# Optimization experiments

Measured on AMD Instinct MI355X. Metric: run time of the kernel, lower is better.

## Reference

```python
import jax, jax.numpy as jnp
import numpy as np
import math

EMBED_DIM = 768
NUM_HEADS = 12
MLP_HIDDEN = int(EMBED_DIM * 2.0)
LN_EPS = 1e-6


def _complex_linear(r, i, wr, wi, br, bi):
    # (r + i*j) @ (wr + wi*j)^T + (br + bi*j)
    out_r = r @ wr.T - i @ wi.T + br
    out_i = r @ wi.T + i @ wr.T + bi
    return out_r, out_i


def _complex_layernorm(r, i, gamma, beta):
    # magnitude-based LN over feature dim; gamma/beta: [F, 2]
    mag = jnp.sqrt(r * r + i * i + LN_EPS)           # [..., F]
    mean = mag.mean(axis=-1, keepdims=True)
    var = ((mag - mean) ** 2).mean(axis=-1, keepdims=True)  # unbiased=False
    norm_mag = (mag - mean) / jnp.sqrt(var + LN_EPS)
    scale = norm_mag / (mag + LN_EPS)
    r_n = r * scale
    i_n = i * scale
    return gamma[..., 0] * r_n + beta[..., 0], gamma[..., 1] * i_n + beta[..., 1]


def setup_inputs() -> dict:
    key = jax.random.key(0)
    ks = jax.random.split(key, 12)
    B, N, E, H = 2, 2048, EMBED_DIM, MLP_HIDDEN
    std_qkv = math.sqrt(2.0 / (E + 3 * E))
    std_proj = math.sqrt(2.0 / (E + E))
    std_fc1 = math.sqrt(2.0 / (E + H))
    std_fc2 = math.sqrt(2.0 / (H + E))
    inp = {
        "x": jax.random.normal(ks[0], (B, N, 2 * E), dtype=jnp.float32),
        "norm1_gamma": 1.0 + 0.1 * jax.random.normal(ks[1], (E, 2), dtype=jnp.float32),
        "norm1_beta": 0.1 * jax.random.normal(ks[2], (E, 2), dtype=jnp.float32),
        "qkv_wr": std_qkv * jax.random.normal(ks[3], (3 * E, E), dtype=jnp.float32),
        "qkv_wi": std_qkv * jax.random.normal(ks[4], (3 * E, E), dtype=jnp.float32),
        "qkv_br": jnp.zeros((3 * E,), dtype=jnp.float32),
        "qkv_bi": jnp.zeros((3 * E,), dtype=jnp.float32),
        "proj_wr": std_proj * jax.random.normal(ks[5], (E, E), dtype=jnp.float32),
        "proj_wi": std_proj * jax.random.normal(ks[6], (E, E), dtype=jnp.float32),
        "proj_br": jnp.zeros((E,), dtype=jnp.float32),
        "proj_bi": jnp.zeros((E,), dtype=jnp.float32),
        "norm2_gamma": 1.0 + 0.1 * jax.random.normal(ks[7], (E, 2), dtype=jnp.float32),
        "norm2_beta": 0.1 * jax.random.normal(ks[8], (E, 2), dtype=jnp.float32),
        "fc1_wr": std_fc1 * jax.random.normal(ks[9], (H, E), dtype=jnp.float32),
        "fc1_wi": std_fc1 * jax.random.normal(ks[10], (H, E), dtype=jnp.float32),
        "fc1_br": jnp.zeros((H,), dtype=jnp.float32),
        "fc1_bi": jnp.zeros((H,), dtype=jnp.float32),
        "fc2_wr": std_fc2 * jax.random.normal(ks[11], (E, H), dtype=jnp.float32),
        "fc2_wi": std_fc2 * jax.random.normal(jax.random.fold_in(key, 99), (E, H), dtype=jnp.float32),
        "fc2_br": jnp.zeros((E,), dtype=jnp.float32),
        "fc2_bi": jnp.zeros((E,), dtype=jnp.float32),
    }
    return inp


def reference(x, norm1_gamma, norm1_beta, qkv_wr, qkv_wi, qkv_br, qkv_bi,
              proj_wr, proj_wi, proj_br, proj_bi, norm2_gamma, norm2_beta,
              fc1_wr, fc1_wi, fc1_br, fc1_bi, fc2_wr, fc2_wi, fc2_br, fc2_bi):
    B, N, _ = x.shape
    E, nH = EMBED_DIM, NUM_HEADS
    hd = E // nH
    xc = x.reshape(B, N, E, 2)
    xr, xi = xc[..., 0], xc[..., 1]

    # --- attention branch ---
    nr, ni = _complex_layernorm(xr, xi, norm1_gamma, norm1_beta)
    qkv_r, qkv_i = _complex_linear(nr, ni, qkv_wr, qkv_wi, qkv_br, qkv_bi)  # [B,N,3E]
    # split to [3, B, nH, N, hd]
    def split_heads(t):
        return t.reshape(B, N, 3, nH, hd).transpose(2, 0, 3, 1, 4)
    qkv_r = split_heads(qkv_r)
    qkv_i = split_heads(qkv_i)
    qr, kr, vr = qkv_r[0], qkv_r[1], qkv_r[2]
    qi, ki, vi = qkv_i[0], qkv_i[1], qkv_i[2]

    # complex attention scores: q * conj-free formulation per source
    attn_real = jnp.einsum('bhqd,bhkd->bhqk', qr, kr) + jnp.einsum('bhqd,bhkd->bhqk', qi, ki)
    attn_imag = jnp.einsum('bhqd,bhkd->bhqk', qr, ki) - jnp.einsum('bhqd,bhkd->bhqk', qi, kr)
    attn_mag = jnp.sqrt(attn_real ** 2 + attn_imag ** 2 + 1e-8) / math.sqrt(hd)
    attn_w = jax.nn.softmax(attn_mag, axis=-1)
    out_r = jnp.einsum('bhqk,bhkd->bhqd', attn_w, vr)
    out_i = jnp.einsum('bhqk,bhkd->bhqd', attn_w, vi)
    # [B,nH,N,hd] -> [B,N,E]
    out_r = out_r.transpose(0, 2, 1, 3).reshape(B, N, E)
    out_i = out_i.transpose(0, 2, 1, 3).reshape(B, N, E)
    pr, pi = _complex_linear(out_r, out_i, proj_wr, proj_wi, proj_br, proj_bi)
    xr = xr + pr
    xi = xi + pi

    # --- MLP branch ---
    nr2, ni2 = _complex_layernorm(xr, xi, norm2_gamma, norm2_beta)
    h_r, h_i = _complex_linear(nr2, ni2, fc1_wr, fc1_wi, fc1_br, fc1_bi)
    h_r = jax.nn.gelu(h_r, approximate=False)
    h_i = jax.nn.gelu(h_i, approximate=False)
    m_r, m_i = _complex_linear(h_r, h_i, fc2_wr, fc2_wi, fc2_br, fc2_bi)
    xr = xr + m_r
    xi = xi + m_i

    return jnp.stack([xr, xi], axis=-1).reshape(B, N, 2 * E)
```

## Files before the change

### kernel.cpp

```cpp
#include <hip/hip_runtime.h>
#include <cmath>

typedef __bf16 bf16;
typedef __bf16 bf16x8 __attribute__((ext_vector_type(8)));
typedef __bf16 bf16x4 __attribute__((ext_vector_type(4)));
typedef float  f32x4  __attribute__((ext_vector_type(4)));
typedef unsigned int u32x4 __attribute__((ext_vector_type(4)));

#define MFMA16(a, b, c) __builtin_amdgcn_mfma_f32_16x16x32_bf16((a), (b), (c), 0, 0, 0)
#define LOG2E 1.44269504088896f

static __device__ __forceinline__ void gl_lds16(const void* g, void* l) {
    __builtin_amdgcn_global_load_lds((const __attribute__((address_space(1))) void*)g,
                                     (__attribute__((address_space(3))) void*)l, 16, 0, 0);
}

static __device__ __forceinline__ bf16x8 bneg8(bf16x8 x) {
    u32x4 u = __builtin_bit_cast(u32x4, x);
    u = u ^ 0x80008000u;
    return __builtin_bit_cast(bf16x8, u);
}

static __device__ __forceinline__ f32x4 zero4() {
    return f32x4{0.0f, 0.0f, 0.0f, 0.0f};
}

__global__ void fill_kernel(float* p, float v, int n) {
    for (int i = blockIdx.x * blockDim.x + threadIdx.x; i < n; i += gridDim.x * blockDim.x)
        p[i] = v;
}

struct Cvt8 {
    const float* s[8];
    bf16* d[8];
    int boff[9];
};
__global__ __launch_bounds__(256) void cvt8_kernel(Cvt8 c) {
    int blk = blockIdx.x;
    int seg = 0;
#pragma unroll
    for (int k = 0; k < 7; ++k)
        if (blk >= c.boff[k + 1]) seg = k + 1;
    const int local = blk - c.boff[seg];
    const int i = local * 1024 + threadIdx.x * 4;
    const float4 v = *(const float4*)(c.s[seg] + i);
    bf16x4 o;
    o[0] = (bf16)v.x; o[1] = (bf16)v.y; o[2] = (bf16)v.z; o[3] = (bf16)v.w;
    *(bf16x4*)(c.d[seg] + i) = o;
}

template <bool ILV>
__global__ __launch_bounds__(256) void cln_kernel(
    const float* __restrict__ xa, const float* __restrict__ xb,
    const float* __restrict__ gamma, const float* __restrict__ beta,
    bf16* __restrict__ nr, bf16* __restrict__ ni) {
    __shared__ float red[4];
    const int t = threadIdx.x;
    const size_t base = (size_t)blockIdx.x * 768;

    float r[3], im[3], mg[3];
#pragma unroll
    for (int j = 0; j < 3; ++j) {
        const int f = t + j * 256;
        if (ILV) {
            const float2 v = ((const float2*)xa)[base + f];
            r[j] = v.x;
            im[j] = v.y;
        } else {
            r[j] = xa[base + f];
            im[j] = xb[base + f];
        }
        mg[j] = __builtin_amdgcn_sqrtf(r[j] * r[j] + im[j] * im[j] + 1e-6f);
    }
    float s = mg[0] + mg[1] + mg[2];
#pragma unroll
    for (int m = 32; m >= 1; m >>= 1) s += __shfl_xor(s, m);
    if ((t & 63) == 0) red[t >> 6] = s;
    __syncthreads();
    const float mean = (red[0] + red[1] + red[2] + red[3]) * (1.0f / 768.0f);
    __syncthreads();

    float v2 = 0.0f;
#pragma unroll
    for (int j = 0; j < 3; ++j) {
        const float d = mg[j] - mean;
        v2 += d * d;
    }
#pragma unroll
    for (int m = 32; m >= 1; m >>= 1) v2 += __shfl_xor(v2, m);
    if ((t & 63) == 0) red[t >> 6] = v2;
    __syncthreads();
    const float var = (red[0] + red[1] + red[2] + red[3]) * (1.0f / 768.0f);
    const float rstd = rsqrtf(var + 1e-6f);

#pragma unroll
    for (int j = 0; j < 3; ++j) {
        const int f = t + j * 256;
        const float sc = (mg[j] - mean) * rstd / (mg[j] + 1e-6f);
        nr[base + f] = (bf16)(gamma[2 * f] * (r[j] * sc) + beta[2 * f]);
        ni[base + f] = (bf16)(gamma[2 * f + 1] * (im[j] * sc) + beta[2 * f + 1]);
    }
}

template <int BM, int BN, int MODE, int OCC>
__global__ __launch_bounds__(256, OCC) void cgemm_kernel(
    const bf16* __restrict__ Ar, const bf16* __restrict__ Ai,
    const bf16* __restrict__ Wr, const bf16* __restrict__ Wi,
    const float* __restrict__ br, const float* __restrict__ bi,
    const float* __restrict__ resr, const float* __restrict__ resi,
    float* __restrict__ outFr, float* __restrict__ outFi,
    bf16* __restrict__ outBr, bf16* __restrict__ outBi,
    int N, int K) {
    constexpr int MR = BM / 32;
    constexpr int NR = BN / 32;
    constexpr int ASEG = BM / 8;
    constexpr int NSEG = (BM + BN) / 8;
    constexpr int SPW = NSEG / 4;

    __shared__ __align__(16) bf16 sA[2][BM][64];
    __shared__ __align__(16) bf16 sB[2][BN][64];

    const int tid = threadIdx.x;
    const int wave = tid >> 6, lane = tid & 63;
    const int lg = lane >> 4, lr = lane & 15;

    const int nwgx = gridDim.x;
    int wg = blockIdx.y * nwgx + blockIdx.x;
    const int cpx = (nwgx * gridDim.y) >> 3;
    wg = (wg & 7) * cpx + (wg >> 3);
    const int row0 = (wg % nwgx) * BM, col0 = (wg / nwgx) * BN;

    const int wm = (wave >> 1) * (BM / 2), wn = (wave & 1) * (BN / 2);

    const int srow = lane >> 3;
    const int schunk = (lane & 7) ^ srow;
    const int spl = schunk >> 2;
    const int sc8 = (schunk & 3) * 8;

    auto issue = [&](int buf, int kt) {
#pragma unroll
        for (int s = 0; s < SPW; ++s) {
            const int id = wave * SPW + s;
            if (id < ASEG) {
                const int row = id * 8 + srow;
                gl_lds16((spl ? Ai : Ar) + (size_t)(row0 + row) * K + kt + sc8,
                         &sA[buf][id * 8][0]);
            } else {
                const int row = (id - ASEG) * 8 + srow;
                gl_lds16((spl ? Wi : Wr) + (size_t)(col0 + row) * K + kt + sc8,
                         &sB[buf][(id - ASEG) * 8][0]);
            }
        }
    };

    f32x4 accr[MR][NR], acci[MR][NR];
#pragma unroll
    for (int a = 0; a < MR; ++a)
#pragma unroll
        for (int b2 = 0; b2 < NR; ++b2) {
            accr[a][b2] = zero4();
            acci[a][b2] = zero4();
        }

    issue(0, 0);

    const int KT = K / 32;
    for (int kt = 0; kt < KT; ++kt) {
        const int buf = kt & 1;
        if (kt + 1 < KT) {
            issue(buf ^ 1, (kt + 1) * 32);
            __builtin_amdgcn_sched_barrier(0);
            if constexpr (SPW == 8)
                asm volatile("s_waitcnt vmcnt(8)" ::: "memory");
            else if constexpr (SPW == 6)
                asm volatile("s_waitcnt vmcnt(6)" ::: "memory");
            else
                asm volatile("s_waitcnt vmcnt(0)" ::: "memory");
        } else {
            asm volatile("s_waitcnt vmcnt(0)" ::: "memory");
        }
        __builtin_amdgcn_sched_barrier(0);
        __builtin_amdgcn_s_barrier();
        __builtin_amdgcn_sched_barrier(0);

        __builtin_amdgcn_s_setprio(1);
        bf16x8 ar[MR], ai[MR], an[MR];
#pragma unroll
        for (int mt = 0; mt < MR; ++mt) {
            const int rr = wm + mt * 16 + lr;
            const int slr = lg ^ (rr & 7);
            const int sli = (4 + lg) ^ (rr & 7);
            ar[mt] = *(const bf16x8*)(&sA[buf][rr][slr * 8]);
            ai[mt] = *(const bf16x8*)(&sA[buf][rr][sli * 8]);
            an[mt] = bneg8(ai[mt]);
        }
#pragma unroll
        for (int nt = 0; nt < NR; ++nt) {
            const int rr = wn + nt * 16 + lr;
            const int slr = lg ^ (rr & 7);
            const int sli = (4 + lg) ^ (rr & 7);
            const bf16x8 br8 = *(const bf16x8*)(&sB[buf][rr][slr * 8]);
            const bf16x8 bi8 = *(const bf16x8*)(&sB[buf][rr][sli * 8]);
#pragma unroll
            for (int mt = 0; mt < MR; ++mt) {
                accr[mt][nt] = MFMA16(ar[mt], br8, accr[mt][nt]);
                accr[mt][nt] = MFMA16(an[mt], bi8, accr[mt][nt]);
                acci[mt][nt] = MFMA16(ar[mt], bi8, acci[mt][nt]);
                acci[mt][nt] = MFMA16(ai[mt], br8, acci[mt][nt]);
            }
        }
        __builtin_amdgcn_s_setprio(0);

        if (kt + 1 < KT) {
            __builtin_amdgcn_sched_barrier(0);
            __builtin_amdgcn_s_barrier();
            __builtin_amdgcn_sched_barrier(0);
        }
    }

#pragma unroll
    for (int nt = 0; nt < NR; ++nt) {
        const int col = col0 + wn + nt * 16 + lr;
        const float bre = br[col], bie = bi[col];
#pragma unroll
        for (int mt = 0; mt < MR; ++mt) {
#pragma unroll
            for (int j = 0; j < 4; ++j) {
                const int row = row0 + wm + mt * 16 + lg * 4 + j;
                float vr = accr[mt][nt][j] + bre;
                float vi = acci[mt][nt][j] + bie;
                const size_t o = (size_t)row * N + col;
                if (MODE == 0) {
                    outBr[o] = (bf16)vr;
                    outBi[o] = (bf16)vi;
                } else if (MODE == 1) {
                    const float2 rv = ((const float2*)resr)[(size_t)row * 768 + col];
                    outFr[o] = rv.x + vr;
                    outFi[o] = rv.y + vi;
                } else if (MODE == 2) {
                    vr = 0.5f * vr * (1.0f + erff(vr * 0.70710678118654752f));
                    vi = 0.5f * vi * (1.0f + erff(vi * 0.70710678118654752f));
                    outBr[o] = (bf16)vr;
                    outBi[o] = (bf16)vi;
                } else {
                    const size_t ro = (size_t)row * 768 + col;
                    outFr[(size_t)row * 1536 + 2 * col]     = resr[ro] + vr;
                    outFr[(size_t)row * 1536 + 2 * col + 1] = resi[ro] + vi;
                }
            }
        }
    }
}

__global__ __launch_bounds__(256) void vtrans_kernel(
    const bf16* __restrict__ qkvr, const bf16* __restrict__ qkvi,
    bf16* __restrict__ vtr, bf16* __restrict__ vti) {
    __shared__ bf16 sr[64][65];
    __shared__ bf16 si[64][65];
    const int t = threadIdx.x;
    const int nb = blockIdx.x, h = blockIdx.y, b = blockIdx.z;
    const size_t ld = 2304;
    const bf16* srcr = qkvr + (size_t)(b * 2048 + nb * 64) * ld + 1536 + h * 64;
    const bf16* srci = qkvi + (size_t)(b * 2048 + nb * 64) * ld + 1536 + h * 64;
#pragma unroll
    for (int j = 0; j < 16; ++j) {
        const int idx = t + 256 * j;
        const int n = idx >> 6, d = idx & 63;
        sr[n][d] = srcr[(size_t)n * ld + d];
        si[n][d] = srci[(size_t)n * ld + d];
    }
    __syncthreads();
    bf16* dstr = vtr + (size_t)(b * 12 + h) * 64 * 2048 + nb * 64;
    bf16* dsti = vti + (size_t)(b * 12 + h) * 64 * 2048 + nb * 64;
#pragma unroll
    for (int j = 0; j < 16; ++j) {
        const int idx = t + 256 * j;
        const int d = idx >> 6, n = idx & 63;
        dstr[(size_t)d * 2048 + n] = sr[n][d];
        dsti[(size_t)d * 2048 + n] = si[n][d];
    }
}

__global__ __launch_bounds__(256, 3) void cattn_kernel(
    const bf16* __restrict__ qkvr, const bf16* __restrict__ qkvi,
    const bf16* __restrict__ vtr, const bf16* __restrict__ vti,
    bf16* __restrict__ aor, bf16* __restrict__ aoi) {
    __shared__ __align__(16) bf16 sK[2][2][32][64];
    __shared__ __align__(16) bf16 sV[2][64][64];
    __shared__ __align__(16) bf16 sP[4][16][40];

    const int tid = threadIdx.x;
    const int w = tid >> 6, lane = tid & 63;
    const int lg = lane >> 4, lr = lane & 15;
    const int qb = blockIdx.x, h = blockIdx.y, b = blockIdx.z;
    const int ld = 2304;

    const int s_krow = lane >> 3;
    const int s_kch8 = ((lane & 7) ^ s_krow) * 8;
    const int s_vlog = (lane & 7) ^ s_krow;
    const int s_vpl = s_vlog >> 2;
    const int s_vk8 = (s_vlog & 3) * 8;

    const bf16* kbase0 = qkvr + (size_t)b * 2048 * ld + 768 + h * 64;
    const bf16* kbase1 = qkvi + (size_t)b * 2048 * ld + 768 + h * 64;
    const bf16* vbase = (s_vpl ? vti : vtr) + (size_t)(b * 12 + h) * 64 * 2048;

    const bf16* kp0 = kbase0 + (size_t)(w * 8 + s_krow) * ld + s_kch8;
    const bf16* kp1 = kbase1 + (size_t)(w * 8 + s_krow) * ld + s_kch8;
    const bf16* vp0 = vbase + (size_t)(w * 8 + s_krow) * 2048 + s_vk8;
    const bf16* vp1 = vbase + (size_t)((4 + w) * 8 + s_krow) * 2048 + s_vk8;

    auto stage = [&](int buf) {
        gl_lds16(kp0, &sK[buf][0][w * 8][0]);
        gl_lds16(kp1, &sK[buf][1][w * 8][0]);
        gl_lds16(vp0, &sV[buf][w * 8][0]);
        gl_lds16(vp1, &sV[buf][(4 + w) * 8][0]);
        kp0 += 32 * ld;
        kp1 += 32 * ld;
        vp0 += 32;
        vp1 += 32;
    };

    stage(0);

    const size_t qoff = (size_t)(b * 2048 + qb * 64 + w * 16 + lr) * ld + h * 64;
    bf16x8 aqr[2], aqi[2];
#pragma unroll
    for (int ks = 0; ks < 2; ++ks) {
        aqr[ks] = *(const bf16x8*)(qkvr + qoff + ks * 32 + lg * 8);
        aqi[ks] = *(const bf16x8*)(qkvi + qoff + ks * 32 + lg * 8);
    }

    f32x4 our[4], oui[4];
#pragma unroll
    for (int d = 0; d < 4; ++d) {
        our[d] = zero4();
        oui[d] = zero4();
    }
    const float C1 = 0.125f * LOG2E;
    float mrun = -1e30f, lrun = 0.0f;
    float thr2 = -1.0f;
    float mC2 = 0.0f;

    for (int kt = 0; kt < 64; ++kt) {
        const int cur = kt & 1;
        if (kt < 63) {
            stage(cur ^ 1);
            __builtin_amdgcn_sched_barrier(0);
            asm volatile("s_waitcnt vmcnt(4)" ::: "memory");
        } else {
            asm volatile("s_waitcnt vmcnt(0)" ::: "memory");
        }
        __builtin_amdgcn_sched_barrier(0);
        __builtin_amdgcn_s_barrier();
        __builtin_amdgcn_sched_barrier(0);

        f32x4 str[2], sti[2];
        str[0] = zero4(); str[1] = zero4();
        sti[0] = zero4(); sti[1] = zero4();
        __builtin_amdgcn_s_setprio(1);
#pragma unroll
        for (int t = 0; t < 2; ++t) {
#pragma unroll
            for (int ks = 0; ks < 2; ++ks) {
                const int ch = ((ks << 2) | lg) ^ (lr & 7);
                const bf16x8 kr8 = *(const bf16x8*)(&sK[cur][0][t * 16 + lr][ch * 8]);
                const bf16x8 ki8 = *(const bf16x8*)(&sK[cur][1][t * 16 + lr][ch * 8]);
                const bf16x8 kn8 = bneg8(kr8);
                str[t] = MFMA16(kr8, aqr[ks], str[t]);
                str[t] = MFMA16(ki8, aqi[ks], str[t]);
                sti[t] = MFMA16(ki8, aqr[ks], sti[t]);
                sti[t] = MFMA16(kn8, aqi[ks], sti[t]);
            }
        }
        __builtin_amdgcn_s_setprio(0);

        float v[8];
        float vmax = 0.0f;
#pragma unroll
        for (int t = 0; t < 2; ++t)
#pragma unroll
            for (int j = 0; j < 4; ++j) {
                const float sr = str[t][j], si = sti[t][j];
                const float vv = fmaf(sr, sr, fmaf(si, si, 1e-8f));
                v[t * 4 + j] = vv;
                vmax = fmaxf(vmax, vv);
            }
        vmax = fmaxf(vmax, __shfl_xor(vmax, 16));
        vmax = fmaxf(vmax, __shfl_xor(vmax, 32));

        if (!__all(vmax <= thr2)) {
            const float tm = __builtin_amdgcn_sqrtf(vmax) * 0.125f;
            const float mnew = fmaxf(mrun, tm);
            const float corr = __builtin_amdgcn_exp2f((mrun - mnew) * LOG2E);
            float cj[4];
#pragma unroll
            for (int j = 0; j < 4; ++j) cj[j] = __shfl(corr, lg * 4 + j);
#pragma unroll
            for (int d = 0; d < 4; ++d)
#pragma unroll
                for (int j = 0; j < 4; ++j) {
                    our[d][j] *= cj[j];
                    oui[d][j] *= cj[j];
                }
            lrun *= corr;
            mrun = mnew;
            const float m8 = mrun + 8.0f;
            thr2 = 64.0f * m8 * m8;
            mC2 = -mrun * LOG2E;
        }

        float p[8];
        float ls = 0.0f;
#pragma unroll
        for (int i = 0; i < 8; ++i) {
            p[i] = __builtin_amdgcn_exp2f(
                fmaf(__builtin_amdgcn_sqrtf(v[i]), C1, mC2));
            ls += p[i];
        }
        ls += __shfl_xor(ls, 16);
        ls += __shfl_xor(ls, 32);
        lrun += ls;

#pragma unroll
        for (int t = 0; t < 2; ++t) {
            bf16x4 pk;
#pragma unroll
            for (int j = 0; j < 4; ++j) pk[j] = (bf16)p[t * 4 + j];
            *(bf16x4*)(&sP[w][lr][t * 16 + lg * 4]) = pk;
        }
        const bf16x8 pf = *(const bf16x8*)(&sP[w][lr][lg * 8]);

        __builtin_amdgcn_s_setprio(1);
#pragma unroll
        for (int d = 0; d < 4; ++d) {
            const int slr = lg ^ (lr & 7);
            const int sli = (4 + lg) ^ (lr & 7);
            const bf16x8 vr8 = *(const bf16x8*)(&sV[cur][d * 16 + lr][slr * 8]);
            const bf16x8 vi8 = *(const bf16x8*)(&sV[cur][d * 16 + lr][sli * 8]);
            our[d] = MFMA16(pf, vr8, our[d]);
            oui[d] = MFMA16(pf, vi8, oui[d]);
        }
        __builtin_amdgcn_s_setprio(0);

        __builtin_amdgcn_sched_barrier(0);
        __builtin_amdgcn_s_barrier();
        __builtin_amdgcn_sched_barrier(0);
    }

    float linv[4];
#pragma unroll
    for (int j = 0; j < 4; ++j) {
        const float lj = __shfl(lrun, lg * 4 + j);
        linv[j] = __builtin_amdgcn_rcpf(lj);
    }
#pragma unroll
    for (int d = 0; d < 4; ++d)
#pragma unroll
        for (int j = 0; j < 4; ++j) {
            const int row = b * 2048 + qb * 64 + w * 16 + lg * 4 + j;
            const int col = h * 64 + d * 16 + lr;
            aor[(size_t)row * 768 + col] = (bf16)(our[d][j] * linv[j]);
            aoi[(size_t)row * 768 + col] = (bf16)(oui[d][j] * linv[j]);
        }
}

extern "C" void kernel_launch(void* const* d_in, const int* in_sizes, int n_in,
                              void* d_out, int out_size, void* d_ws, size_t ws_size,
                              hipStream_t stream) {
    const float* x      = (const float*)d_in[0];
    const float* n1g    = (const float*)d_in[1];
    const float* n1b    = (const float*)d_in[2];
    const float* qkvwr  = (const float*)d_in[3];
    const float* qkvwi  = (const float*)d_in[4];
    const float* qkvbr  = (const float*)d_in[5];
    const float* qkvbi  = (const float*)d_in[6];
    const float* projwr = (const float*)d_in[7];
    const float* projwi = (const float*)d_in[8];
    const float* projbr = (const float*)d_in[9];
    const float* projbi = (const float*)d_in[10];
    const float* n2g    = (const float*)d_in[11];
    const float* n2b    = (const float*)d_in[12];
    const float* fc1wr  = (const float*)d_in[13];
    const float* fc1wi  = (const float*)d_in[14];
    const float* fc1br  = (const float*)d_in[15];
    const float* fc1bi  = (const float*)d_in[16];
    const float* fc2wr  = (const float*)d_in[17];
    const float* fc2wi  = (const float*)d_in[18];
    const float* fc2br  = (const float*)d_in[19];
    const float* fc2bi  = (const float*)d_in[20];

    const int M = 4096, E = 768, E3 = 2304, HH = 1536;

    char* base = (char*)d_ws;
    size_t off = 0;
    auto alloc = [&](size_t bytes) -> void* {
        void* p = base + off;
        off += (bytes + 255) & ~(size_t)255;
        return p;
    };
    float* xr2 = (float*)alloc((size_t)M * E * 4);
    float* xi2 = (float*)alloc((size_t)M * E * 4);
    bf16* nr   = (bf16*)alloc((size_t)M * E * 2);
    bf16* ni   = (bf16*)alloc((size_t)M * E * 2);
    bf16* wqr  = (bf16*)alloc((size_t)E3 * E * 2);
    bf16* wqi  = (bf16*)alloc((size_t)E3 * E * 2);
    bf16* wpr  = (bf16*)alloc((size_t)E * E * 2);
    bf16* wpi  = (bf16*)alloc((size_t)E * E * 2);
    bf16* w1r  = (bf16*)alloc((size_t)HH * E * 2);
    bf16* w1i  = (bf16*)alloc((size_t)HH * E * 2);
    bf16* w2r  = (bf16*)alloc((size_t)E * HH * 2);
    bf16* w2i  = (bf16*)alloc((size_t)E * HH * 2);
    bf16* qkr  = (bf16*)alloc((size_t)M * E3 * 2);
    bf16* qki  = (bf16*)alloc((size_t)M * E3 * 2);
    bf16* vtr  = (bf16*)alloc((size_t)24 * 64 * 2048 * 2);
    bf16* vti  = (bf16*)alloc((size_t)24 * 64 * 2048 * 2);
    bf16* aor  = (bf16*)alloc((size_t)M * E * 2);
    bf16* aoi  = (bf16*)alloc((size_t)M * E * 2);
    bf16* hr   = (bf16*)alloc((size_t)M * HH * 2);
    bf16* hi   = (bf16*)alloc((size_t)M * HH * 2);

    if (off > ws_size) {
        fill_kernel<<<1024, 256, 0, stream>>>((float*)d_out, 1.0e9f, out_size);
        return;
    }

    Cvt8 c;
    c.s[0] = qkvwr; c.d[0] = wqr;
    c.s[1] = qkvwi; c.d[1] = wqi;
    c.s[2] = projwr; c.d[2] = wpr;
    c.s[3] = projwi; c.d[3] = wpi;
    c.s[4] = fc1wr; c.d[4] = w1r;
    c.s[5] = fc1wi; c.d[5] = w1i;
    c.s[6] = fc2wr; c.d[6] = w2r;
    c.s[7] = fc2wi; c.d[7] = w2i;
    const int nseg[8] = {E3 * E, E3 * E, E * E, E * E, HH * E, HH * E, E * HH, E * HH};
    int cum = 0;
    for (int k = 0; k < 8; ++k) {
        c.boff[k] = cum;
        cum += nseg[k] / 1024;
    }
    c.boff[8] = cum;
    cvt8_kernel<<<cum, 256, 0, stream>>>(c);

    cln_kernel<true><<<M, 256, 0, stream>>>(x, nullptr, n1g, n1b, nr, ni);
    cgemm_kernel<128, 128, 0, 2><<<dim3(32, 18), 256, 0, stream>>>(
        nr, ni, wqr, wqi, qkvbr, qkvbi, nullptr, nullptr, nullptr, nullptr,
        qkr, qki, E3, E);
    vtrans_kernel<<<dim3(32, 12, 2), 256, 0, stream>>>(qkr, qki, vtr, vti);
    cattn_kernel<<<dim3(32, 12, 2), 256, 0, stream>>>(qkr, qki, vtr, vti, aor, aoi);
    cgemm_kernel<128, 64, 1, 3><<<dim3(32, 12), 256, 0, stream>>>(
        aor, aoi, wpr, wpi, projbr, projbi, x, nullptr, xr2, xi2, nullptr, nullptr,
        E, E);
    cln_kernel<false><<<M, 256, 0, stream>>>(xr2, xi2, n2g, n2b, nr, ni);
    cgemm_kernel<128, 128, 2, 2><<<dim3(32, 12), 256, 0, stream>>>(
        nr, ni, w1r, w1i, fc1br, fc1bi, nullptr, nullptr, nullptr, nullptr,
        hr, hi, HH, E);
    cgemm_kernel<128, 64, 3, 3><<<dim3(32, 12), 256, 0, stream>>>(
        hr, hi, w2r, w2i, fc2br, fc2bi, xr2, xi2, (float*)d_out, nullptr,
        nullptr, nullptr, E, HH);
}
```

Measured before the change: 371.1 us.

## Software-pipeline PV MFMA one tile behind QK in attention; fast GELU; drop setprio

The attention kernel now runs the P·V MFMAs for the previous key tile right after the current QK MFMAs, using a triple-buffered V tile in LDS. This lets the matrix work overlap the softmax exp/sqrt section of the same iteration. The GELU epilogue in the GEMM replaces erff with a tanh-style sigmoid approximation built from exp2 and rcp, which changes numerics slightly. The s_setprio calls around the GEMM main loop are removed. The cost is more LDS per block, which may reduce occupancy, and a small deviation from exact GELU.

```diff
diff --git a/kernel.cpp b/kernel.cpp
--- a/kernel.cpp
+++ b/kernel.cpp
@@ -183,7 +183,6 @@
         __builtin_amdgcn_s_barrier();
         __builtin_amdgcn_sched_barrier(0);
 
-        __builtin_amdgcn_s_setprio(1);
         bf16x8 ar[MR], ai[MR], an[MR];
 #pragma unroll
         for (int mt = 0; mt < MR; ++mt) {
@@ -209,7 +208,6 @@
                 acci[mt][nt] = MFMA16(ai[mt], br8, acci[mt][nt]);
             }
         }
-        __builtin_amdgcn_s_setprio(0);
 
         if (kt + 1 < KT) {
             __builtin_amdgcn_sched_barrier(0);
@@ -238,8 +236,12 @@
                     outFr[o] = rv.x + vr;
                     outFi[o] = rv.y + vi;
                 } else if (MODE == 2) {
-                    vr = 0.5f * vr * (1.0f + erff(vr * 0.70710678118654752f));
-                    vi = 0.5f * vi * (1.0f + erff(vi * 0.70710678118654752f));
+                    const float t2r = fmaf(vr * vr, 0.044715f, 1.0f);
+                    const float er = __builtin_amdgcn_exp2f(vr * t2r * 2.3022082f);
+                    vr = vr - vr * __builtin_amdgcn_rcpf(er + 1.0f);
+                    const float t2i = fmaf(vi * vi, 0.044715f, 1.0f);
+                    const float ei = __builtin_amdgcn_exp2f(vi * t2i * 2.3022082f);
+                    vi = vi - vi * __builtin_amdgcn_rcpf(ei + 1.0f);
                     outBr[o] = (bf16)vr;
                     outBi[o] = (bf16)vi;
                 } else {
@@ -286,7 +288,7 @@
     const bf16* __restrict__ vtr, const bf16* __restrict__ vti,
     bf16* __restrict__ aor, bf16* __restrict__ aoi) {
     __shared__ __align__(16) bf16 sK[2][2][32][64];
-    __shared__ __align__(16) bf16 sV[2][64][64];
+    __shared__ __align__(16) bf16 sV[3][64][64];
     __shared__ __align__(16) bf16 sP[4][16][40];
 
     const int tid = threadIdx.x;
@@ -310,18 +312,18 @@
     const bf16* vp0 = vbase + (size_t)(w * 8 + s_krow) * 2048 + s_vk8;
     const bf16* vp1 = vbase + (size_t)((4 + w) * 8 + s_krow) * 2048 + s_vk8;
 
-    auto stage = [&](int buf) {
-        gl_lds16(kp0, &sK[buf][0][w * 8][0]);
-        gl_lds16(kp1, &sK[buf][1][w * 8][0]);
-        gl_lds16(vp0, &sV[buf][w * 8][0]);
-        gl_lds16(vp1, &sV[buf][(4 + w) * 8][0]);
+    auto stage = [&](int kb, int vs) {
+        gl_lds16(kp0, &sK[kb][0][w * 8][0]);
+        gl_lds16(kp1, &sK[kb][1][w * 8][0]);
+        gl_lds16(vp0, &sV[vs][w * 8][0]);
+        gl_lds16(vp1, &sV[vs][(4 + w) * 8][0]);
         kp0 += 32 * ld;
         kp1 += 32 * ld;
         vp0 += 32;
         vp1 += 32;
     };
 
-    stage(0);
+    stage(0, 0);
 
     const size_t qoff = (size_t)(b * 2048 + qb * 64 + w * 16 + lr) * ld + h * 64;
     bf16x8 aqr[2], aqi[2];
@@ -342,10 +344,17 @@
     float thr2 = -1.0f;
     float mC2 = 0.0f;
 
+    bf16x8 pfPrev = __builtin_bit_cast(bf16x8, u32x4{0u, 0u, 0u, 0u});
+    int vcur = 0, vlast = 0;
+    const int slr = lg ^ (lr & 7);
+    const int sli = (4 + lg) ^ (lr & 7);
+
     for (int kt = 0; kt < 64; ++kt) {
-        const int cur = kt & 1;
+        const int kcur = kt & 1;
+        int vnext = vcur + 1;
+        if (vnext == 3) vnext = 0;
         if (kt < 63) {
-            stage(cur ^ 1);
+            stage(kcur ^ 1, vnext);
             __builtin_amdgcn_sched_barrier(0);
             asm volatile("s_waitcnt vmcnt(4)" ::: "memory");
         } else {
@@ -364,13 +373,22 @@
 #pragma unroll
             for (int ks = 0; ks < 2; ++ks) {
                 const int ch = ((ks << 2) | lg) ^ (lr & 7);
-                const bf16x8 kr8 = *(const bf16x8*)(&sK[cur][0][t * 16 + lr][ch * 8]);
-                const bf16x8 ki8 = *(const bf16x8*)(&sK[cur][1][t * 16 + lr][ch * 8]);
+                const bf16x8 kr8 = *(const bf16x8*)(&sK[kcur][0][t * 16 + lr][ch * 8]);
+                const bf16x8 ki8 = *(const bf16x8*)(&sK[kcur][1][t * 16 + lr][ch * 8]);
                 const bf16x8 kn8 = bneg8(kr8);
                 str[t] = MFMA16(kr8, aqr[ks], str[t]);
                 str[t] = MFMA16(ki8, aqi[ks], str[t]);
                 sti[t] = MFMA16(ki8, aqr[ks], sti[t]);
                 sti[t] = MFMA16(kn8, aqi[ks], sti[t]);
+            }
+        }
+        if (kt > 0) {
+#pragma unroll
+            for (int d = 0; d < 4; ++d) {
+                const bf16x8 vr8 = *(const bf16x8*)(&sV[vlast][d * 16 + lr][slr * 8]);
+                const bf16x8 vi8 = *(const bf16x8*)(&sV[vlast][d * 16 + lr][sli * 8]);
+                our[d] = MFMA16(pfPrev, vr8, our[d]);
+                oui[d] = MFMA16(pfPrev, vi8, oui[d]);
             }
         }
         __builtin_amdgcn_s_setprio(0);
@@ -429,23 +447,22 @@
             for (int j = 0; j < 4; ++j) pk[j] = (bf16)p[t * 4 + j];
             *(bf16x4*)(&sP[w][lr][t * 16 + lg * 4]) = pk;
         }
-        const bf16x8 pf = *(const bf16x8*)(&sP[w][lr][lg * 8]);
-
-        __builtin_amdgcn_s_setprio(1);
-#pragma unroll
-        for (int d = 0; d < 4; ++d) {
-            const int slr = lg ^ (lr & 7);
-            const int sli = (4 + lg) ^ (lr & 7);
-            const bf16x8 vr8 = *(const bf16x8*)(&sV[cur][d * 16 + lr][slr * 8]);
-            const bf16x8 vi8 = *(const bf16x8*)(&sV[cur][d * 16 + lr][sli * 8]);
-            our[d] = MFMA16(pf, vr8, our[d]);
-            oui[d] = MFMA16(pf, vi8, oui[d]);
-        }
-        __builtin_amdgcn_s_setprio(0);
+        pfPrev = *(const bf16x8*)(&sP[w][lr][lg * 8]);
+
+        vlast = vcur;
+        vcur = vnext;
 
         __builtin_amdgcn_sched_barrier(0);
         __builtin_amdgcn_s_barrier();
         __builtin_amdgcn_sched_barrier(0);
+    }
+
+#pragma unroll
+    for (int d = 0; d < 4; ++d) {
+        const bf16x8 vr8 = *(const bf16x8*)(&sV[vlast][d * 16 + lr][slr * 8]);
+        const bf16x8 vi8 = *(const bf16x8*)(&sV[vlast][d * 16 + lr][sli * 8]);
+        our[d] = MFMA16(pfPrev, vr8, our[d]);
+        oui[d] = MFMA16(pfPrev, vi8, oui[d]);
     }
 
     float linv[4];
```

Measured after the change: 355.1 us. 4.3% less time.
